# Kernel tuning notes

Hardware: AMD Instinct MI355X
Metric: run time of the kernel (lower is better)

Reference implementation:

```python
import jax, jax.numpy as jnp
import numpy as np

EPS = 1e-5
TAU = 0.1

def _bn(x, g, b):
    # BatchNorm1d in training mode: batch statistics (biased variance)
    mu = jnp.mean(x, axis=0, keepdims=True)
    var = jnp.var(x, axis=0, keepdims=True)
    return (x - mu) * jax.lax.rsqrt(var + EPS) * g + b

def setup_inputs():
    key = jax.random.key(0)
    ks = jax.random.split(key, 8)
    B, D, H, L, P, C, ND, NP = 32768, 2048, 1024, 384, 192, 10, 2, 2
    s = 0.02
    u = jax.random.uniform(ks[7], (B, NP), minval=1e-6, maxval=1.0 - 1e-6)
    return {
        'x': jax.random.normal(ks[0], (B, D), dtype=jnp.float32),
        'W_pre': jax.random.normal(ks[1], (H, D), dtype=jnp.float32) * s,
        'b_pre': jnp.zeros((H,), jnp.float32),
        'g_pre': jnp.ones((H,), jnp.float32),
        'be_pre': jnp.zeros((H,), jnp.float32),
        'W_disc': jax.random.normal(ks[2], (L, H), dtype=jnp.float32) * s,
        'b_disc': jnp.zeros((L,), jnp.float32),
        'g_disc': jnp.ones((L,), jnp.float32),
        'be_disc': jnp.zeros((L,), jnp.float32),
        'W_dfc': jax.random.normal(ks[3], (ND, L), dtype=jnp.float32) * s,
        'b_dfc': jnp.zeros((ND,), jnp.float32),
        'W_sw': jax.random.normal(ks[4], (NP, L), dtype=jnp.float32) * s,
        'b_sw': jnp.zeros((NP,), jnp.float32),
        'W1': jax.random.normal(ks[5], (NP, P, H), dtype=jnp.float32) * s,
        'b1': jnp.zeros((NP, P), jnp.float32),
        'W2': jax.random.normal(ks[6], (NP, C, P), dtype=jnp.float32) * s,
        'b2': jnp.zeros((NP, C), jnp.float32),
        'gumbel_noise': -jnp.log(-jnp.log(u)),
    }

def reference(x, W_pre, b_pre, g_pre, be_pre, W_disc, b_disc, g_disc, be_disc,
              W_dfc, b_dfc, W_sw, b_sw, W1, b1, W2, b2, gumbel_noise):
    # pre_classifier: Linear + BN + ReLU
    feature = jax.nn.relu(_bn(x @ W_pre.T + b_pre, g_pre, be_pre))
    # GRL is identity in forward
    dp = jax.nn.relu(_bn(feature @ W_disc.T + b_disc, g_disc, be_disc))
    dom = dp @ W_dfc.T + b_dfc                      # [B, num_domains]
    sw = jax.nn.relu(dp @ W_sw.T + b_sw)            # [B, n_partition]
    gum = jax.nn.softmax((sw + gumbel_noise) / TAU, axis=-1)  # soft gumbel-softmax
    idx = jnp.argmax(gum, axis=-1)                  # [B] routing decision
    # compute both (tiny) experts densely, then select per sample (faithful math,
    # avoids per-sample gather of full weight matrices)
    h_all = jax.nn.relu(jnp.einsum('bd,epd->bep', feature, W1) + b1)  # [B,E,P]
    o_all = jnp.einsum('bep,ecp->bec', h_all, W2) + b2                # [B,E,C]
    out = jnp.take_along_axis(o_all, idx[:, None, None], axis=1)[:, 0]  # [B,C]
    # original: sum_p gum[b,p] * stacked (stacked has one entry) == out * sum(gum)
    cop = out * jnp.sum(gum, axis=-1, keepdims=True)
    return cop, dom, idx
```

## Files before the change

kernel.cpp:

```cpp
#include <hip/hip_runtime.h>
#include <math.h>

#define kB 32768
#define kD 2048
#define kH 1024
#define kL 384
#define kP 192
#define kC 10
#define kNP 2
#define kND 2
#define kNCAT 768
#define kTAU 0.1f
#define kEPS 1e-5f
#define NPART 512
#define SCALE 64.0f
#define INV_SC2 (1.0f / 4096.0f)

typedef _Float16 f16x8 __attribute__((ext_vector_type(8)));
typedef _Float16 f16x4 __attribute__((ext_vector_type(4)));
typedef float f32x4 __attribute__((ext_vector_type(4)));

#define WAITVM0   asm volatile("s_waitcnt vmcnt(0)" ::: "memory")
#define WAITVM4   asm volatile("s_waitcnt vmcnt(4)" ::: "memory")
#define WAITLGKM0 asm volatile("s_waitcnt lgkmcnt(0)" ::: "memory")
#define SB0       __builtin_amdgcn_sched_barrier(0)
#define BAR       __builtin_amdgcn_s_barrier()

__device__ __forceinline__ void gll16(const unsigned short* g, unsigned short* l)
{
    __builtin_amdgcn_global_load_lds(
        (const __attribute__((address_space(1))) unsigned int*)g,
        (__attribute__((address_space(3))) unsigned int*)l, 16, 0, 0);
}

__device__ __host__ __forceinline__ int wkey(int r)
{
    return (r & 1) | ((r & 2) << 1) | ((r & 4) >> 1);
}

__global__ __launch_bounds__(256)
void split_pack(const float* __restrict__ in, unsigned short* __restrict__ out, int K)
{
    const int row = blockIdx.x;
    const int t = threadIdx.x;
    const int s = wkey(row & 7);
    const float* ir = in + (size_t)row * K;
    unsigned short* orow = out + (size_t)row * (K * 2);
    for (int k0 = t * 4; k0 < K; k0 += 1024) {
        const float4 v = *(const float4*)&ir[k0];
        const float a0 = v.x * SCALE, a1 = v.y * SCALE, a2 = v.z * SCALE, a3 = v.w * SCALE;
        const _Float16 h0 = (_Float16)a0, h1 = (_Float16)a1, h2 = (_Float16)a2, h3 = (_Float16)a3;
        const _Float16 l0 = (_Float16)(a0 - (float)h0), l1 = (_Float16)(a1 - (float)h1);
        const _Float16 l2 = (_Float16)(a2 - (float)h2), l3 = (_Float16)(a3 - (float)h3);
        const f16x4 hi = {h0, h1, h2, h3};
        const f16x4 lo = {l0, l1, l2, l3};
        const int kb = k0 >> 5, kk = k0 & 31;
        const int c = kk >> 3, off = kk & 7;
        *(f16x4*)&orow[kb * 64 + ((c ^ s) << 3) + off]       = hi;
        *(f16x4*)&orow[kb * 64 + (((c ^ 4) ^ s) << 3) + off] = lo;
    }
}

template<int KDIM, bool BN>
__global__ __launch_bounds__(256, 3)
void gemm_fused(const float* __restrict__ Afp,
                const unsigned short* __restrict__ Bpk,
                const float* __restrict__ bnsc, const float* __restrict__ bnsh,
                float* __restrict__ C, const int N, const int gridX,
                float* __restrict__ psum, float* __restrict__ psumsq, const int statN)
{
    constexpr int NKB = KDIM / 32;
    __shared__ __align__(16) unsigned short As_[128 * 64];
    __shared__ __align__(16) unsigned short Bs_[128 * 64];
    __shared__ float sScL[BN ? KDIM : 4];
    __shared__ float sShL[BN ? KDIM : 4];

    const int t = threadIdx.x;
    const int lane = t & 63;
    const int w = t >> 6;
    const int wr = w >> 1, wc = w & 1;
    const int lr = lane & 15, lg = lane >> 4;
    const int ca = (lg ^ wkey(lane & 7)) * 8;

    const int nwg = gridDim.x;
    const int chunk = nwg >> 3;
    const int bid = blockIdx.x;
    const int logical = (bid & 7) * chunk + (bid >> 3);
    const int bx = logical % gridX, by = logical / gridX;
    const int m0 = by * 128, n0 = bx * 128;

    const int arow = t >> 1;
    const int akh = t & 1;
    const int skey = wkey(arow & 7);
    const int c0 = akh * 2, c1 = akh * 2 + 1;
    const float* aSrc = Afp + (size_t)(m0 + arow) * KDIM + akh * 16;

    const size_t bstride = (size_t)NKB * 64;
    const unsigned short* bG[4];
    int bLoff[4];
#pragma unroll
    for (int it = 0; it < 4; ++it) {
        const int Q = (w * 4 + it) * 64 + lane;
        bG[it] = Bpk + (size_t)(n0 + (Q >> 3)) * bstride + (Q & 7) * 8;
        bLoff[it] = (w * 4 + it) * 512;
    }

    f32x4 acc[4][4];
#pragma unroll
    for (int mi = 0; mi < 4; ++mi)
#pragma unroll
        for (int ni = 0; ni < 4; ++ni) acc[mi][ni] = (f32x4){0.f, 0.f, 0.f, 0.f};

    float4 av[4];

    auto issueA = [&](int kb) {
        const int kt = kb * 32;
#pragma unroll
        for (int j = 0; j < 4; ++j)
            av[j] = *(const float4*)&aSrc[kt + j * 4];
    };

    auto gllB = [&](int kb) {
#pragma unroll
        for (int it = 0; it < 4; ++it)
            gll16(bG[it] + (size_t)kb * 64, &Bs_[bLoff[it]]);
    };

    auto writeA = [&](int tile) {
        const int kt = tile * 32 + akh * 16;
        float v[16];
#pragma unroll
        for (int j = 0; j < 4; ++j) {
            float4 a = av[j];
            if constexpr (BN) {
                const float4 sc = *(const float4*)&sScL[kt + j * 4];
                const float4 sh = *(const float4*)&sShL[kt + j * 4];
                a.x = fmaxf(fmaf(a.x, sc.x, sh.x), 0.f);
                a.y = fmaxf(fmaf(a.y, sc.y, sh.y), 0.f);
                a.z = fmaxf(fmaf(a.z, sc.z, sh.z), 0.f);
                a.w = fmaxf(fmaf(a.w, sc.w, sh.w), 0.f);
            } else {
                a.x *= SCALE; a.y *= SCALE; a.z *= SCALE; a.w *= SCALE;
            }
            v[j * 4 + 0] = a.x; v[j * 4 + 1] = a.y;
            v[j * 4 + 2] = a.z; v[j * 4 + 3] = a.w;
        }
        f16x8 hi[2], lo[2];
#pragma unroll
        for (int h = 0; h < 2; ++h)
#pragma unroll
            for (int i = 0; i < 8; ++i) {
                const float x = v[h * 8 + i];
                const _Float16 hh = (_Float16)x;
                hi[h][i] = hh;
                lo[h][i] = (_Float16)(x - (float)hh);
            }
        unsigned short* dst = &As_[arow * 64];
        *(f16x8*)&dst[(c0 ^ skey) * 8]       = hi[0];
        *(f16x8*)&dst[(c1 ^ skey) * 8]       = hi[1];
        *(f16x8*)&dst[((c0 ^ 4) ^ skey) * 8] = lo[0];
        *(f16x8*)&dst[((c1 ^ 4) ^ skey) * 8] = lo[1];
    };

    if constexpr (BN) {
        for (int i = t; i < KDIM / 4; i += 256) {
            ((float4*)sScL)[i] = ((const float4*)bnsc)[i];
            ((float4*)sShL)[i] = ((const float4*)bnsh)[i];
        }
        __syncthreads();
    }
    issueA(0);

    for (int s = 0; s < NKB; ++s) {
        const bool pf = (s + 1 < NKB);
        BAR;
        WAITVM0;
        SB0;
        writeA(s);
        gllB(s);
        SB0;
        if (pf) issueA(s + 1);
        SB0;
        if (pf) { WAITVM4; } else { WAITVM0; }
        WAITLGKM0;
        SB0;
        BAR;

        f16x8 bh[4], bl[4];
#pragma unroll
        for (int ni = 0; ni < 4; ++ni) {
            const unsigned short* bb = &Bs_[(wc * 64 + ni * 16 + lr) * 64];
            bh[ni] = *(const f16x8*)&bb[ca];
            bl[ni] = *(const f16x8*)&bb[ca ^ 32];
        }
#pragma unroll
        for (int mi = 0; mi < 4; ++mi) {
            const unsigned short* ab = &As_[(wr * 64 + mi * 16 + lr) * 64];
            const f16x8 ah = *(const f16x8*)&ab[ca];
            const f16x8 al = *(const f16x8*)&ab[ca ^ 32];
#pragma unroll
            for (int ni = 0; ni < 4; ++ni)
                acc[mi][ni] = __builtin_amdgcn_mfma_f32_16x16x32_f16(ah, bh[ni], acc[mi][ni], 0, 0, 0);
#pragma unroll
            for (int ni = 0; ni < 4; ++ni)
                acc[mi][ni] = __builtin_amdgcn_mfma_f32_16x16x32_f16(ah, bl[ni], acc[mi][ni], 0, 0, 0);
#pragma unroll
            for (int ni = 0; ni < 4; ++ni)
                acc[mi][ni] = __builtin_amdgcn_mfma_f32_16x16x32_f16(al, bh[ni], acc[mi][ni], 0, 0, 0);
        }
    }

#pragma unroll
    for (int mi = 0; mi < 4; ++mi)
#pragma unroll
        for (int j = 0; j < 4; ++j) {
            const int row = m0 + wr * 64 + mi * 16 + lg * 4 + j;
            float* cr = C + (size_t)row * N + n0 + wc * 64 + lr;
#pragma unroll
            for (int ni = 0; ni < 4; ++ni) cr[ni * 16] = acc[mi][ni][j];
        }

#pragma unroll
    for (int ni = 0; ni < 4; ++ni) {
        float s = 0.f, sq = 0.f;
#pragma unroll
        for (int mi = 0; mi < 4; ++mi)
#pragma unroll
            for (int j = 0; j < 4; ++j) {
                const float v = acc[mi][ni][j];
                s += v;
                sq = fmaf(v, v, sq);
            }
        s  += __shfl_xor(s, 16);  s  += __shfl_xor(s, 32);
        sq += __shfl_xor(sq, 16); sq += __shfl_xor(sq, 32);
        const int col = n0 + wc * 64 + ni * 16 + lr;
        if (lane < 16 && col < statN) {
            psum[(size_t)(by * 2 + wr) * statN + col]   = s;
            psumsq[(size_t)(by * 2 + wr) * statN + col] = sq;
        }
    }
}

__global__ __launch_bounds__(256)
void colstat_finalize(const float* __restrict__ psum, const float* __restrict__ psumsq,
                      int ncols, const float* __restrict__ g, const float* __restrict__ be,
                      float* __restrict__ scale, float* __restrict__ shift,
                      float inv_sc, float outsc)
{
    const int c = blockIdx.x * 256 + threadIdx.x;
    if (c >= ncols) return;
    float s = 0.f, sq = 0.f;
    for (int i = 0; i < NPART; ++i) {
        s  += psum[(size_t)i * ncols + c];
        sq += psumsq[(size_t)i * ncols + c];
    }
    const float mup = s * (1.f / kB);
    const float var = (sq * (1.f / kB) - mup * mup) * inv_sc * inv_sc;
    const float scl = outsc * g[c] * rsqrtf(var + kEPS) * inv_sc;
    scale[c] = scl;
    shift[c] = fmaf(-mup, scl, outsc * be[c]);
}

__global__ __launch_bounds__(256)
void tail_kernel(const float* __restrict__ Z2,
                 const float* __restrict__ scale2, const float* __restrict__ shift2,
                 const float* __restrict__ W_dfc, const float* __restrict__ b_dfc,
                 const float* __restrict__ W_sw, const float* __restrict__ b_sw,
                 const float* __restrict__ b1, const float* __restrict__ W2,
                 const float* __restrict__ b2, const float* __restrict__ noise,
                 float* __restrict__ out)
{
    __shared__ float sWdfc[kND * kL];
    __shared__ float sWsw[kNP * kL];
    __shared__ float sW2[kNP * kC * kP];
    __shared__ float sb1[kNP * kP];
    __shared__ float sScale[kL];
    __shared__ float sShift[kL];
    const int t = threadIdx.x;
    for (int i = t; i < kND * kL; i += 256) sWdfc[i] = W_dfc[i];
    for (int i = t; i < kNP * kL; i += 256) sWsw[i] = W_sw[i];
    for (int i = t; i < kNP * kC * kP; i += 256) sW2[i] = W2[i];
    for (int i = t; i < kNP * kP; i += 256) sb1[i] = b1[i];
    for (int i = t; i < kL; i += 256) { sScale[i] = scale2[i]; sShift[i] = shift2[i]; }
    __syncthreads();

    const int lane = t & 63;
    const int b = blockIdx.x * 4 + (t >> 6);
    const float* z = Z2 + (size_t)b * kNCAT;

    float d0 = 0.f, d1 = 0.f, s0 = 0.f, s1 = 0.f;
#pragma unroll
    for (int j = 0; j < 6; ++j) {
        const int k = lane + j * 64;
        const float dp = fmaxf(fmaf(z[k], sScale[k], sShift[k]), 0.f);
        d0 = fmaf(dp, sWdfc[k],      d0);
        d1 = fmaf(dp, sWdfc[kL + k], d1);
        s0 = fmaf(dp, sWsw[k],       s0);
        s1 = fmaf(dp, sWsw[kL + k],  s1);
    }
#pragma unroll
    for (int off = 32; off; off >>= 1) {
        d0 += __shfl_xor(d0, off);
        d1 += __shfl_xor(d1, off);
        s0 += __shfl_xor(s0, off);
        s1 += __shfl_xor(s1, off);
    }
    d0 += b_dfc[0];
    d1 += b_dfc[1];

    const float sw0 = fmaxf(s0 + b_sw[0], 0.f);
    const float sw1 = fmaxf(s1 + b_sw[1], 0.f);
    const float l0 = (sw0 + noise[(size_t)b * 2 + 0]) * (1.f / kTAU);
    const float l1 = (sw1 + noise[(size_t)b * 2 + 1]) * (1.f / kTAU);
    const float mx = fmaxf(l0, l1);
    const float e0 = expf(l0 - mx), e1 = expf(l1 - mx);
    const float inv = 1.f / (e0 + e1);
    const float sgum = e0 * inv + e1 * inv;
    const int idx = (l1 > l0) ? 1 : 0;

    const float* zh = z + kL + idx * kP;
    const float h0 = fmaxf(fmaf(zh[lane],       INV_SC2, sb1[idx * kP + lane]),       0.f);
    const float h1 = fmaxf(fmaf(zh[lane + 64],  INV_SC2, sb1[idx * kP + lane + 64]),  0.f);
    const float h2 = fmaxf(fmaf(zh[lane + 128], INV_SC2, sb1[idx * kP + lane + 128]), 0.f);

    float* cop  = out;
    float* dom  = out + (size_t)kB * kC;
    float* idxo = dom + (size_t)kB * kND;

#pragma unroll
    for (int c = 0; c < kC; ++c) {
        const float* wv = &sW2[(idx * kC + c) * kP];
        float oc = h0 * wv[lane] + h1 * wv[lane + 64] + h2 * wv[lane + 128];
#pragma unroll
        for (int off = 32; off; off >>= 1) oc += __shfl_xor(oc, off);
        if (lane == c) cop[(size_t)b * kC + c] = (oc + b2[idx * kC + c]) * sgum;
    }
    if (lane == 0) {
        dom[(size_t)b * 2 + 0] = d0;
        dom[(size_t)b * 2 + 1] = d1;
        idxo[b] = (float)idx;
    }
}

extern "C" void kernel_launch(void* const* d_in, const int* in_sizes, int n_in,
                              void* d_out, int out_size, void* d_ws, size_t ws_size,
                              hipStream_t stream)
{
    const float* x       = (const float*)d_in[0];
    const float* W_pre   = (const float*)d_in[1];
    const float* g_pre   = (const float*)d_in[3];
    const float* be_pre  = (const float*)d_in[4];
    const float* W_disc  = (const float*)d_in[5];
    const float* g_disc  = (const float*)d_in[7];
    const float* be_disc = (const float*)d_in[8];
    const float* W_dfc   = (const float*)d_in[9];
    const float* b_dfc   = (const float*)d_in[10];
    const float* W_sw    = (const float*)d_in[11];
    const float* b_sw    = (const float*)d_in[12];
    const float* W1      = (const float*)d_in[13];
    const float* b1      = (const float*)d_in[14];
    const float* W2      = (const float*)d_in[15];
    const float* b2      = (const float*)d_in[16];
    const float* noise   = (const float*)d_in[17];

    char* wsb = (char*)d_ws;
    unsigned short* Wps = (unsigned short*)wsb;
    unsigned short* Ws2 = (unsigned short*)(wsb + (size_t)1024 * 4096 * 2);
    float* Z1 = (float*)(wsb + (size_t)1024 * 4096 * 2 + (size_t)768 * 2048 * 2);
    float* Z2 = Z1 + (size_t)kB * kH;
    float* psum1  = Z2 + (size_t)kB * kNCAT;
    float* psq1   = psum1 + (size_t)NPART * kH;
    float* psum2  = psq1 + (size_t)NPART * kH;
    float* psq2   = psum2 + (size_t)NPART * kL;
    float* scale1 = psq2 + (size_t)NPART * kL;
    float* shift1 = scale1 + kH;
    float* scale2 = shift1 + kH;
    float* shift2 = scale2 + kL;
    float* out    = (float*)d_out;

    split_pack<<<dim3(kH), 256, 0, stream>>>(W_pre, Wps, kD);
    split_pack<<<dim3(kL), 256, 0, stream>>>(W_disc, Ws2, kH);
    split_pack<<<dim3(kNP * kP), 256, 0, stream>>>(W1, Ws2 + (size_t)kL * (2 * kH), kH);
    gemm_fused<kD, false><<<dim3(8 * 256), 256, 0, stream>>>(
        x, Wps, nullptr, nullptr, Z1, kH, 8, psum1, psq1, kH);
    colstat_finalize<<<dim3(kH / 256), 256, 0, stream>>>(psum1, psq1, kH, g_pre, be_pre,
                                                         scale1, shift1, INV_SC2, SCALE);
    gemm_fused<kH, true><<<dim3(6 * 256), 256, 0, stream>>>(
        Z1, Ws2, scale1, shift1, Z2, kNCAT, 6, psum2, psq2, kL);
    colstat_finalize<<<dim3((kL + 255) / 256), 256, 0, stream>>>(psum2, psq2, kL, g_disc, be_disc,
                                                                 scale2, shift2, INV_SC2, 1.0f);
    tail_kernel<<<dim3(kB / 4), 256, 0, stream>>>(Z2, scale2, shift2, W_dfc, b_dfc,
                                                  W_sw, b_sw, b1, W2, b2, noise, out);
}
```

Baseline: 724.8 us.

## Enlarge GEMM M-tile to 256 rows per workgroup

The fused GEMM tile grows from 128x128 to 256x128. Each thread now loads and splits a full 32-wide row of A, and each wave accumulates 8x4 MFMA tiles instead of 4x4, which halves the grid and the partial-stat count. The aim is to double reuse of each B tile loaded into LDS and cut B global traffic per FLOP. In exchange the kernel needs twice the accumulator registers and A LDS space, with occupancy bounds lowered from 3 to 2 and a deeper vmcnt wait.

```diff
diff --git a/kernel.cpp b/kernel.cpp
--- a/kernel.cpp
+++ b/kernel.cpp
@@ -12,7 +12,7 @@
 #define kNCAT 768
 #define kTAU 0.1f
 #define kEPS 1e-5f
-#define NPART 512
+#define NPART 256
 #define SCALE 64.0f
 #define INV_SC2 (1.0f / 4096.0f)
 
@@ -21,7 +21,7 @@
 typedef float f32x4 __attribute__((ext_vector_type(4)));
 
 #define WAITVM0   asm volatile("s_waitcnt vmcnt(0)" ::: "memory")
-#define WAITVM4   asm volatile("s_waitcnt vmcnt(4)" ::: "memory")
+#define WAITVM8   asm volatile("s_waitcnt vmcnt(8)" ::: "memory")
 #define WAITLGKM0 asm volatile("s_waitcnt lgkmcnt(0)" ::: "memory")
 #define SB0       __builtin_amdgcn_sched_barrier(0)
 #define BAR       __builtin_amdgcn_s_barrier()
@@ -62,7 +62,7 @@
 }
 
 template<int KDIM, bool BN>
-__global__ __launch_bounds__(256, 3)
+__global__ __launch_bounds__(256, 2)
 void gemm_fused(const float* __restrict__ Afp,
                 const unsigned short* __restrict__ Bpk,
                 const float* __restrict__ bnsc, const float* __restrict__ bnsh,
@@ -70,7 +70,7 @@
                 float* __restrict__ psum, float* __restrict__ psumsq, const int statN)
 {
     constexpr int NKB = KDIM / 32;
-    __shared__ __align__(16) unsigned short As_[128 * 64];
+    __shared__ __align__(16) unsigned short As_[256 * 64];
     __shared__ __align__(16) unsigned short Bs_[128 * 64];
     __shared__ float sScL[BN ? KDIM : 4];
     __shared__ float sShL[BN ? KDIM : 4];
@@ -87,13 +87,10 @@
     const int bid = blockIdx.x;
     const int logical = (bid & 7) * chunk + (bid >> 3);
     const int bx = logical % gridX, by = logical / gridX;
-    const int m0 = by * 128, n0 = bx * 128;
-
-    const int arow = t >> 1;
-    const int akh = t & 1;
-    const int skey = wkey(arow & 7);
-    const int c0 = akh * 2, c1 = akh * 2 + 1;
-    const float* aSrc = Afp + (size_t)(m0 + arow) * KDIM + akh * 16;
+    const int m0 = by * 256, n0 = bx * 128;
+
+    const int skey = wkey(t & 7);
+    const float* aSrc = Afp + (size_t)(m0 + t) * KDIM;
 
     const size_t bstride = (size_t)NKB * 64;
     const unsigned short* bG[4];
@@ -105,18 +102,18 @@
         bLoff[it] = (w * 4 + it) * 512;
     }
 
-    f32x4 acc[4][4];
-#pragma unroll
-    for (int mi = 0; mi < 4; ++mi)
+    f32x4 acc[8][4];
+#pragma unroll
+    for (int mi = 0; mi < 8; ++mi)
 #pragma unroll
         for (int ni = 0; ni < 4; ++ni) acc[mi][ni] = (f32x4){0.f, 0.f, 0.f, 0.f};
 
-    float4 av[4];
+    float4 av[8];
 
     auto issueA = [&](int kb) {
         const int kt = kb * 32;
 #pragma unroll
-        for (int j = 0; j < 4; ++j)
+        for (int j = 0; j < 8; ++j)
             av[j] = *(const float4*)&aSrc[kt + j * 4];
     };
 
@@ -127,39 +124,37 @@
     };
 
     auto writeA = [&](int tile) {
-        const int kt = tile * 32 + akh * 16;
-        float v[16];
-#pragma unroll
-        for (int j = 0; j < 4; ++j) {
-            float4 a = av[j];
-            if constexpr (BN) {
-                const float4 sc = *(const float4*)&sScL[kt + j * 4];
-                const float4 sh = *(const float4*)&sShL[kt + j * 4];
-                a.x = fmaxf(fmaf(a.x, sc.x, sh.x), 0.f);
-                a.y = fmaxf(fmaf(a.y, sc.y, sh.y), 0.f);
-                a.z = fmaxf(fmaf(a.z, sc.z, sh.z), 0.f);
-                a.w = fmaxf(fmaf(a.w, sc.w, sh.w), 0.f);
-            } else {
-                a.x *= SCALE; a.y *= SCALE; a.z *= SCALE; a.w *= SCALE;
+        const int kt = tile * 32;
+        unsigned short* dst = &As_[t * 64];
+#pragma unroll
+        for (int h = 0; h < 4; ++h) {
+            float v[8];
+#pragma unroll
+            for (int p = 0; p < 2; ++p) {
+                float4 a = av[h * 2 + p];
+                if constexpr (BN) {
+                    const float4 sc = *(const float4*)&sScL[kt + h * 8 + p * 4];
+                    const float4 sh = *(const float4*)&sShL[kt + h * 8 + p * 4];
+                    a.x = fmaxf(fmaf(a.x, sc.x, sh.x), 0.f);
+                    a.y = fmaxf(fmaf(a.y, sc.y, sh.y), 0.f);
+                    a.z = fmaxf(fmaf(a.z, sc.z, sh.z), 0.f);
+                    a.w = fmaxf(fmaf(a.w, sc.w, sh.w), 0.f);
+                } else {
+                    a.x *= SCALE; a.y *= SCALE; a.z *= SCALE; a.w *= SCALE;
+                }
+                v[p * 4 + 0] = a.x; v[p * 4 + 1] = a.y;
+                v[p * 4 + 2] = a.z; v[p * 4 + 3] = a.w;
             }
-            v[j * 4 + 0] = a.x; v[j * 4 + 1] = a.y;
-            v[j * 4 + 2] = a.z; v[j * 4 + 3] = a.w;
-        }
-        f16x8 hi[2], lo[2];
-#pragma unroll
-        for (int h = 0; h < 2; ++h)
+            f16x8 hi, lo;
 #pragma unroll
             for (int i = 0; i < 8; ++i) {
-                const float x = v[h * 8 + i];
-                const _Float16 hh = (_Float16)x;
-                hi[h][i] = hh;
-                lo[h][i] = (_Float16)(x - (float)hh);
+                const _Float16 hh = (_Float16)v[i];
+                hi[i] = hh;
+                lo[i] = (_Float16)(v[i] - (float)hh);
             }
-        unsigned short* dst = &As_[arow * 64];
-        *(f16x8*)&dst[(c0 ^ skey) * 8]       = hi[0];
-        *(f16x8*)&dst[(c1 ^ skey) * 8]       = hi[1];
-        *(f16x8*)&dst[((c0 ^ 4) ^ skey) * 8] = lo[0];
-        *(f16x8*)&dst[((c1 ^ 4) ^ skey) * 8] = lo[1];
+            *(f16x8*)&dst[((h     ^ skey) << 3)] = hi;
+            *(f16x8*)&dst[(((h^4) ^ skey) << 3)] = lo;
+        }
     };
 
     if constexpr (BN) {
@@ -181,7 +176,7 @@
         SB0;
         if (pf) issueA(s + 1);
         SB0;
-        if (pf) { WAITVM4; } else { WAITVM0; }
+        if (pf) { WAITVM8; } else { WAITVM0; }
         WAITLGKM0;
         SB0;
         BAR;
@@ -194,8 +189,8 @@
             bl[ni] = *(const f16x8*)&bb[ca ^ 32];
         }
 #pragma unroll
-        for (int mi = 0; mi < 4; ++mi) {
-            const unsigned short* ab = &As_[(wr * 64 + mi * 16 + lr) * 64];
+        for (int mi = 0; mi < 8; ++mi) {
+            const unsigned short* ab = &As_[(wr * 128 + mi * 16 + lr) * 64];
             const f16x8 ah = *(const f16x8*)&ab[ca];
             const f16x8 al = *(const f16x8*)&ab[ca ^ 32];
 #pragma unroll
@@ -211,10 +206,10 @@
     }
 
 #pragma unroll
-    for (int mi = 0; mi < 4; ++mi)
+    for (int mi = 0; mi < 8; ++mi)
 #pragma unroll
         for (int j = 0; j < 4; ++j) {
-            const int row = m0 + wr * 64 + mi * 16 + lg * 4 + j;
+            const int row = m0 + wr * 128 + mi * 16 + lg * 4 + j;
             float* cr = C + (size_t)row * N + n0 + wc * 64 + lr;
 #pragma unroll
             for (int ni = 0; ni < 4; ++ni) cr[ni * 16] = acc[mi][ni][j];
@@ -224,7 +219,7 @@
     for (int ni = 0; ni < 4; ++ni) {
         float s = 0.f, sq = 0.f;
 #pragma unroll
-        for (int mi = 0; mi < 4; ++mi)
+        for (int mi = 0; mi < 8; ++mi)
 #pragma unroll
             for (int j = 0; j < 4; ++j) {
                 const float v = acc[mi][ni][j];
@@ -381,11 +376,11 @@
     split_pack<<<dim3(kH), 256, 0, stream>>>(W_pre, Wps, kD);
     split_pack<<<dim3(kL), 256, 0, stream>>>(W_disc, Ws2, kH);
     split_pack<<<dim3(kNP * kP), 256, 0, stream>>>(W1, Ws2 + (size_t)kL * (2 * kH), kH);
-    gemm_fused<kD, false><<<dim3(8 * 256), 256, 0, stream>>>(
+    gemm_fused<kD, false><<<dim3(128 * 8), 256, 0, stream>>>(
         x, Wps, nullptr, nullptr, Z1, kH, 8, psum1, psq1, kH);
     colstat_finalize<<<dim3(kH / 256), 256, 0, stream>>>(psum1, psq1, kH, g_pre, be_pre,
                                                          scale1, shift1, INV_SC2, SCALE);
-    gemm_fused<kH, true><<<dim3(6 * 256), 256, 0, stream>>>(
+    gemm_fused<kH, true><<<dim3(128 * 6), 256, 0, stream>>>(
         Z1, Ws2, scale1, shift1, Z2, kNCAT, 6, psum2, psq2, kL);
     colstat_finalize<<<dim3((kL + 255) / 256), 256, 0, stream>>>(psum2, psq2, kL, g_disc, be_disc,
                                                                  scale2, shift2, INV_SC2, 1.0f);
```

Measured after the change: 726.1 us. No clear change (+0.2%).
